# Performance work log

Hardware: AMD Instinct MI355X
Metric: run time of the kernel (lower is better)

Reference implementation:

```python
import jax, jax.numpy as jnp
import numpy as np
import math

H = 8
D_MODEL = 512
D_K = D_MODEL // H
NEG = -1.0e9


def setup_inputs() -> dict:
    key = jax.random.key(0)
    ks = jax.random.split(key, 10)
    B, S, D = 8, 1024, D_MODEL
    s = 1.0 / math.sqrt(D)
    return {
        "query": jax.random.normal(ks[0], (B, S, D), jnp.float32),
        "key": jax.random.normal(ks[1], (B, S, D), jnp.float32),
        "value": jax.random.normal(ks[2], (B, S, D), jnp.float32),
        "group_prob": jax.random.uniform(ks[3], (B, S, S), jnp.float32),
        "Wq": jax.random.normal(ks[4], (D, D), jnp.float32) * s,
        "Wk": jax.random.normal(ks[5], (D, D), jnp.float32) * s,
        "Wv": jax.random.normal(ks[6], (D, D), jnp.float32) * s,
        "Wh": jax.random.normal(ks[7], (D, D), jnp.float32) * s,
        "bh": jax.random.normal(ks[8], (D,), jnp.float32) * s,
        "mask": jax.random.randint(ks[9], (B, S, S), 0, 2, jnp.int32),
    }


def reference(query, key, value, group_prob, Wq, Wk, Wv, Wh, bh, mask):
    B, S, D = query.shape
    # project and split heads: [B, H, S, d_k]
    def split(x, W):
        return (x @ W.T).reshape(B, S, H, D_K).transpose(0, 2, 1, 3)
    q, k, v = split(query, Wq), split(key, Wk), split(value, Wv)
    scores = jnp.einsum('bhqd,bhkd->bhqk', q, k) / jnp.sqrt(jnp.asarray(D_K, q.dtype))
    # masked_fill where (mask | eye) == 0, i.e. keep mask-allowed or diagonal positions
    eye = jnp.eye(S, dtype=jnp.int32)
    allowed = (mask[:, None, :, :] | eye[None, None, :, :]) != 0  # [B,1,S,S]
    scores = jnp.where(allowed, scores, jnp.asarray(NEG, scores.dtype))
    p_attn = jax.nn.softmax(scores, axis=-1)
    p_attn = p_attn * group_prob[:, None, :, :]  # post-softmax group scaling
    x = jnp.einsum('bhqk,bhkd->bhqd', p_attn, v)
    x = x.transpose(0, 2, 1, 3).reshape(B, S, D)
    return x @ Wh.T + bh
```

## Files before the change

### kernel.cpp

```cpp
#include <hip/hip_runtime.h>
#include <hip/hip_bf16.h>
#include <cstdint>


typedef __attribute__((ext_vector_type(8))) short short8;
typedef __attribute__((ext_vector_type(4))) float f32x4;

__device__ __forceinline__ ushort f2bf(float x) {
    union { __hip_bfloat16 h; ushort u; } v;
    v.h = __float2bfloat16(x);
    return v.u;
}
__device__ __forceinline__ float bf2f(ushort u) {
    union { uint u; float f; } v; v.u = ((uint)u) << 16; return v.f;
}
__device__ __forceinline__ uint cvtpk(float lo, float hi) {
    uint r;
    asm("v_cvt_pk_bf16_f32 %0, %1, %2" : "=v"(r) : "v"(lo), "v"(hi));
    return r;
}
__device__ __forceinline__ f32x4 mfma16(short8 a, short8 b, f32x4 c) {
    return __builtin_amdgcn_mfma_f32_16x16x32_bf16(a, b, c, 0, 0, 0);
}
__device__ __forceinline__ void gl16(const void* g, const void* l) {
    __builtin_amdgcn_global_load_lds(
        (const __attribute__((address_space(1))) uint32_t*)(uintptr_t)g,
        (__attribute__((address_space(3))) uint32_t*)(uint32_t)(uintptr_t)l,
        16, 0, 0);
}

__global__ __launch_bounds__(256)
void prep(const float* __restrict__ q, const float* __restrict__ k,
          const float* __restrict__ v,
          const float* __restrict__ wq, const float* __restrict__ wk,
          const float* __restrict__ wv, const float* __restrict__ wh,
          const int* __restrict__ mask, const float* __restrict__ gp,
          ushort* __restrict__ qb, ushort* __restrict__ kb,
          ushort* __restrict__ vb,
          ushort* __restrict__ wqb, ushort* __restrict__ wkb,
          ushort* __restrict__ wvb, ushort* __restrict__ whb,
          ushort* __restrict__ gmb)
{
    const int bid = blockIdx.x, tid = threadIdx.x;
    if (bid < 8192) {
        size_t i = ((size_t)bid * 256 + tid) * 4;
        int4 m = *(const int4*)(mask + i);
        float4 gg = *(const float4*)(gp + i);
        int kk = (int)(i & 1023), qq = (int)((i >> 10) & 1023);
        uint u01 = cvtpk(gg.x, gg.y), u23 = cvtpk(gg.z, gg.w);
        ushort4 o;
        o.x = (m.x != 0 || qq == kk + 0) ? (ushort)(u01 & 0xffff) : (ushort)0xBF80;
        o.y = (m.y != 0 || qq == kk + 1) ? (ushort)(u01 >> 16)    : (ushort)0xBF80;
        o.z = (m.z != 0 || qq == kk + 2) ? (ushort)(u23 & 0xffff) : (ushort)0xBF80;
        o.w = (m.w != 0 || qq == kk + 3) ? (ushort)(u23 >> 16)    : (ushort)0xBF80;
        *(ushort4*)(gmb + i) = o;
    } else if (bid < 20480) {
        size_t id = ((size_t)(bid - 8192) * 256 + tid) * 4;
        int t = (int)(id >> 22);
        size_t off = id & 4194303;
        const float* s = (t == 0) ? q : (t == 1) ? k : v;
        ushort* d = (t == 0) ? qb : (t == 1) ? kb : vb;
        float4 x = *(const float4*)(s + off);
        uint2 o; o.x = cvtpk(x.x, x.y); o.y = cvtpk(x.z, x.w);
        *(uint2*)(d + off) = o;
    } else {
        size_t id = ((size_t)(bid - 20480) * 256 + tid) * 4;
        int t = (int)(id >> 18);
        size_t off = id & 262143;
        const float* s = (t == 0) ? wq : (t == 1) ? wk : (t == 2) ? wv : wh;
        ushort* d = (t == 0) ? wqb : (t == 1) ? wkb : (t == 2) ? wvb : whb;
        float4 x = *(const float4*)(s + off);
        uint2 o; o.x = cvtpk(x.x, x.y); o.y = cvtpk(x.z, x.w);
        *(uint2*)(d + off) = o;
    }
}

__global__ __launch_bounds__(256, 2)
void gemm3(const ushort* __restrict__ qb, const ushort* __restrict__ kb,
           const ushort* __restrict__ vb,
           const ushort* __restrict__ Wqb, const ushort* __restrict__ Wkb,
           const ushort* __restrict__ Wvb,
           ushort* __restrict__ q_ws, ushort* __restrict__ k_ws,
           ushort* __restrict__ vT)
{
    __shared__ __attribute__((aligned(16))) ushort As[8192];
    __shared__ __attribute__((aligned(16))) ushort Bs[8192];

    const int z = blockIdx.z;
    const ushort* A = (z == 0) ? qb : (z == 1) ? kb : Wvb;
    const ushort* B = (z == 0) ? Wqb : (z == 1) ? Wkb : vb;
    const int mt = (z == 2) ? blockIdx.y : blockIdx.x;
    const int nt = (z == 2) ? blockIdx.x : blockIdx.y;
    const int m0 = mt * 128, n0 = nt * 128;
    const int tid = threadIdx.x, lane = tid & 63, wave = tid >> 6;
    const int l15 = lane & 15, g = lane >> 4;
    const int wm = wave >> 1, wn = wave & 1;

    const int cb = (lane & 7) << 4;
    int soff[4];
    #pragma unroll
    for (int it = 0; it < 4; ++it) {
        int r = (it * 4 + wave) * 8 + (lane >> 3);
        soff[it] = r * 1024 + (cb ^ ((r & 7) << 4));
    }
    const char* Ab = (const char*)A + (size_t)m0 * 1024;
    const char* Bb = (const char*)B + (size_t)n0 * 1024;

    const int sw = (l15 & 7) << 4;
    const int c0 = (g * 16) ^ sw;
    const int c1 = (64 + g * 16) ^ sw;

    f32x4 acc[4][4];
    #pragma unroll
    for (int i = 0; i < 4; ++i)
        #pragma unroll
        for (int j = 0; j < 4; ++j) acc[i][j] = (f32x4){0.f, 0.f, 0.f, 0.f};

    for (int ks = 0; ks < 8; ++ks) {
        const int kof = ks * 128;
        #pragma unroll
        for (int it = 0; it < 4; ++it) {
            gl16(Ab + soff[it] + kof, (const char*)As + (it * 4 + wave) * 1024);
            gl16(Bb + soff[it] + kof, (const char*)Bs + (it * 4 + wave) * 1024);
        }
        __syncthreads();
        #pragma unroll
        for (int kk = 0; kk < 2; ++kk) {
            const int cc = kk ? c1 : c0;
            short8 af[4], bf[4];
            #pragma unroll
            for (int i = 0; i < 4; ++i)
                af[i] = *(const short8*)((const char*)As + (wm * 64 + i * 16 + l15) * 128 + cc);
            #pragma unroll
            for (int j = 0; j < 4; ++j)
                bf[j] = *(const short8*)((const char*)Bs + (wn * 64 + j * 16 + l15) * 128 + cc);
            #pragma unroll
            for (int i = 0; i < 4; ++i)
                #pragma unroll
                for (int j = 0; j < 4; ++j)
                    acc[i][j] = mfma16(af[i], bf[j], acc[i][j]);
        }
        __syncthreads();
    }

    #pragma unroll
    for (int i = 0; i < 4; ++i) {
        #pragma unroll
        for (int j = 0; j < 4; ++j) {
            #pragma unroll
            for (int r = 0; r < 4; ++r) {
                int mm = m0 + wm * 64 + i * 16 + g * 4 + r;
                int nn = n0 + wn * 64 + j * 16 + l15;
                float val = acc[i][j][r];
                if (z == 0) {
                    val *= 0.18033688f;
                    int b = mm >> 10, s = mm & 1023, h = nn >> 6, dk = nn & 63;
                    q_ws[((((size_t)(b * 8 + h)) << 10) + s) * 64 + dk] = f2bf(val);
                } else if (z == 1) {
                    int b = mm >> 10, s = mm & 1023, h = nn >> 6, dk = nn & 63;
                    k_ws[((((size_t)(b * 8 + h)) << 10) + s) * 64 + dk] = f2bf(val);
                } else {
                    int h = mm >> 6, d = mm & 63, b = nn >> 10, s = nn & 1023;
                    vT[(((size_t)(b * 8 + h) * 64 + d) << 10) + s] = f2bf(val);
                }
            }
        }
    }
}

__global__ __launch_bounds__(256, 2)
void gemm_o(const ushort* __restrict__ Xh, const ushort* __restrict__ Whb,
            const float* __restrict__ bias, float* __restrict__ out)
{
    __shared__ __attribute__((aligned(16))) ushort As[8192];
    __shared__ __attribute__((aligned(16))) ushort Bs[8192];

    const int m0 = blockIdx.x * 128, n0 = blockIdx.y * 128;
    const int tid = threadIdx.x, lane = tid & 63, wave = tid >> 6;
    const int l15 = lane & 15, g = lane >> 4;
    const int wm = wave >> 1, wn = wave & 1;
    const int bb = m0 >> 10, s0 = m0 & 1023;

    const int cb = (lane & 7) << 4;
    int aoff[4], boff[4];
    #pragma unroll
    for (int it = 0; it < 4; ++it) {
        int r = (it * 4 + wave) * 8 + (lane >> 3);
        int swz = cb ^ ((r & 7) << 4);
        aoff[it] = ((bb * 8) * 1024 + s0 + r) * 128 + swz;
        boff[it] = (n0 + r) * 1024 + swz;
    }
    const int sw = (l15 & 7) << 4;
    const int c0 = (g * 16) ^ sw;
    const int c1 = (64 + g * 16) ^ sw;

    f32x4 acc[4][4];
    #pragma unroll
    for (int i = 0; i < 4; ++i)
        #pragma unroll
        for (int j = 0; j < 4; ++j) acc[i][j] = (f32x4){0.f, 0.f, 0.f, 0.f};

    for (int ks = 0; ks < 8; ++ks) {
        #pragma unroll
        for (int it = 0; it < 4; ++it) {
            gl16((const char*)Xh + aoff[it] + ks * 131072,
                 (const char*)As + (it * 4 + wave) * 1024);
            gl16((const char*)Whb + boff[it] + ks * 128,
                 (const char*)Bs + (it * 4 + wave) * 1024);
        }
        __syncthreads();
        #pragma unroll
        for (int kk = 0; kk < 2; ++kk) {
            const int cc = kk ? c1 : c0;
            short8 af[4], bf[4];
            #pragma unroll
            for (int i = 0; i < 4; ++i)
                af[i] = *(const short8*)((const char*)As + (wm * 64 + i * 16 + l15) * 128 + cc);
            #pragma unroll
            for (int j = 0; j < 4; ++j)
                bf[j] = *(const short8*)((const char*)Bs + (wn * 64 + j * 16 + l15) * 128 + cc);
            #pragma unroll
            for (int i = 0; i < 4; ++i)
                #pragma unroll
                for (int j = 0; j < 4; ++j)
                    acc[i][j] = mfma16(af[i], bf[j], acc[i][j]);
        }
        __syncthreads();
    }

    float bv[4];
    #pragma unroll
    for (int j = 0; j < 4; ++j) bv[j] = bias[n0 + wn * 64 + j * 16 + l15];

    #pragma unroll
    for (int i = 0; i < 4; ++i)
        #pragma unroll
        for (int j = 0; j < 4; ++j)
            #pragma unroll
            for (int r = 0; r < 4; ++r) {
                int mm = m0 + wm * 64 + i * 16 + g * 4 + r;
                int nn = n0 + wn * 64 + j * 16 + l15;
                out[(size_t)mm * 512 + nn] = acc[i][j][r] + bv[j];
            }
}

__device__ __forceinline__ void softmax16(const short8 gc0, const short8 gc1,
                                          const f32x4 (&s4)[4], float& lsum,
                                          uint4& u0, uint4& u1)
{
    float p[16], gv[16];
    #pragma unroll
    for (int c = 0; c < 2; ++c) {
        const short8 gc = c ? gc1 : gc0;
        #pragma unroll
        for (int j = 0; j < 8; ++j) {
            const int jj = c * 8 + j;
            const int t4 = 2 * c + (j >> 2), r = j & 3;
            float gvv = bf2f((ushort)gc[j]);
            gv[jj] = gvv;
            p[jj] = exp2f((gvv >= 0.f) ? s4[t4][r] : -1.0e9f);
        }
    }
    lsum += (((p[0] + p[1]) + (p[2] + p[3])) + ((p[4] + p[5]) + (p[6] + p[7])))
          + (((p[8] + p[9]) + (p[10] + p[11])) + ((p[12] + p[13]) + (p[14] + p[15])));
    u0.x = cvtpk(p[0] * gv[0],  p[1] * gv[1]);
    u0.y = cvtpk(p[2] * gv[2],  p[3] * gv[3]);
    u0.z = cvtpk(p[4] * gv[4],  p[5] * gv[5]);
    u0.w = cvtpk(p[6] * gv[6],  p[7] * gv[7]);
    u1.x = cvtpk(p[8] * gv[8],  p[9] * gv[9]);
    u1.y = cvtpk(p[10] * gv[10], p[11] * gv[11]);
    u1.z = cvtpk(p[12] * gv[12], p[13] * gv[13]);
    u1.w = cvtpk(p[14] * gv[14], p[15] * gv[15]);
}

#define TILE_BODY(T, CUR, GCA0, GCA1, GCB0, GCB1, GNA0, GNA1, GNB0, GNB1)      \
  do {                                                                         \
    if ((T) < 15) {                                                            \
        GNA0 = *(const short8*)(gmpA + ((T) + 1) * 64 + g * 8);                \
        GNA1 = *(const short8*)(gmpA + ((T) + 1) * 64 + 32 + g * 8);           \
        GNB0 = *(const short8*)(gmpB + ((T) + 1) * 64 + g * 8);                \
        GNB1 = *(const short8*)(gmpB + ((T) + 1) * 64 + 32 + g * 8);           \
        const char* kp_ = Kpb + (size_t)((T) + 1) * 8192;                      \
        const char* vp_ = Vpb + (size_t)((T) + 1) * 128;                       \
        char* kd_ = (char*)&kv[(CUR) ^ 1][0][0] + wave * 4096;                 \
        char* vd_ = (char*)&kv[(CUR) ^ 1][1][0] + wave * 4096;                 \
        _Pragma("unroll")                                                      \
        for (int i_ = 0; i_ < 4; ++i_) {                                       \
            gl16(kp_ + koff[i_], kd_ + i_ * 1024);                             \
            gl16(vp_ + voff[i_], vd_ + i_ * 1024);                             \
        }                                                                      \
        asm volatile("s_waitcnt vmcnt(12)" ::: "memory");                      \
    } else {                                                                   \
        asm volatile("s_waitcnt vmcnt(0)" ::: "memory");                       \
    }                                                                          \
    __builtin_amdgcn_s_barrier();                                              \
    __builtin_amdgcn_sched_barrier(0);                                         \
    {                                                                          \
        const char* kbuf_ = (const char*)&kv[CUR][0][0];                       \
        const char* vbuf_ = (const char*)&kv[CUR][1][0];                       \
        f32x4 sA_[4], sB_[4];                                                  \
        __builtin_amdgcn_s_setprio(1);                                         \
        _Pragma("unroll")                                                      \
        for (int t4_ = 0; t4_ < 4; ++t4_) {                                    \
            const char* ka_ = kbuf_ + (t4_ * 16 + l15) * 128;                  \
            short8 k0_ = *(const short8*)(ka_ + c0);                           \
            short8 k1_ = *(const short8*)(ka_ + c1);                           \
            f32x4 za_ = (f32x4){0.f, 0.f, 0.f, 0.f};                           \
            za_ = mfma16(k0_, qa0, za_);                                       \
            za_ = mfma16(k1_, qa1, za_);                                       \
            sA_[t4_] = za_;                                                    \
            f32x4 zb_ = (f32x4){0.f, 0.f, 0.f, 0.f};                           \
            zb_ = mfma16(k0_, qb0, zb_);                                       \
            zb_ = mfma16(k1_, qb1, zb_);                                       \
            sB_[t4_] = zb_;                                                    \
        }                                                                      \
        __builtin_amdgcn_s_setprio(0);                                         \
        union { uint4 u; short8 s; } paA0_, paA1_, paB0_, paB1_;               \
        softmax16(GCA0, GCA1, sA_, lsA, paA0_.u, paA1_.u);                     \
        softmax16(GCB0, GCB1, sB_, lsB, paB0_.u, paB1_.u);                     \
        __builtin_amdgcn_s_setprio(1);                                         \
        _Pragma("unroll")                                                      \
        for (int td_ = 0; td_ < 4; ++td_) {                                    \
            const char* va_ = vbuf_ + (td_ * 16 + l15) * 128;                  \
            short8 v0_ = *(const short8*)(va_ + c0);                           \
            short8 v1_ = *(const short8*)(va_ + c1);                           \
            otA[td_] = mfma16(v0_, paA0_.s, otA[td_]);                         \
            otA[td_] = mfma16(v1_, paA1_.s, otA[td_]);                         \
            otB[td_] = mfma16(v0_, paB0_.s, otB[td_]);                         \
            otB[td_] = mfma16(v1_, paB1_.s, otB[td_]);                         \
        }                                                                      \
        __builtin_amdgcn_s_setprio(0);                                         \
    }                                                                          \
    __builtin_amdgcn_s_barrier();                                              \
  } while (0)

__global__ __launch_bounds__(128, 2)
void attn(const ushort* __restrict__ Qh, const ushort* __restrict__ Kh,
          const ushort* __restrict__ Vt, const ushort* __restrict__ gm,
          ushort* __restrict__ xo)
{
    __shared__ __attribute__((aligned(16))) ushort kv[2][2][4096];

    const int w = blockIdx.x;
    const int bh = w & 63, qt = w >> 6;
    const int tid = threadIdx.x, wave = tid >> 6, lane = tid & 63;
    const int l15 = lane & 15, g = lane >> 4;
    const int q0 = qt * 64 + wave * 32;
    const int b = bh >> 3;

    const char* Kpb = (const char*)(Kh + (size_t)bh * 65536);
    const char* Vpb = (const char*)(Vt + (size_t)bh * 65536);
    const ushort* QpA = Qh + ((size_t)bh * 1024 + q0 + l15) * 64;
    const ushort* QpB = QpA + 1024;
    const ushort* gmpA = gm + ((size_t)b * 1024 + q0 + l15) * 1024;
    const ushort* gmpB = gmpA + 16384;

    const short8 qa0 = *(const short8*)(QpA + g * 8);
    const short8 qa1 = *(const short8*)(QpA + 32 + g * 8);
    const short8 qb0 = *(const short8*)(QpB + g * 8);
    const short8 qb1 = *(const short8*)(QpB + 32 + g * 8);

    const int cbk = ((lane & 7) << 4) ^ ((lane >> 3) << 4);
    int koff[4], voff[4];
    #pragma unroll
    for (int i = 0; i < 4; ++i) {
        int p = (wave * 4 + i) * 8 + (lane >> 3);
        int gk = (p & 3) + 4 * ((p >> 4) & 1) + 8 * ((p >> 2) & 3) + 32 * (p >> 5);
        koff[i] = gk * 128 + cbk;
        voff[i] = p * 2048 + cbk;
    }

    const int sw = (l15 & 7) << 4;
    const int c0 = (g * 16) ^ sw;
    const int c1 = (64 + g * 16) ^ sw;

    f32x4 otA[4], otB[4];
    #pragma unroll
    for (int t = 0; t < 4; ++t) {
        otA[t] = (f32x4){0.f, 0.f, 0.f, 0.f};
        otB[t] = (f32x4){0.f, 0.f, 0.f, 0.f};
    }
    float lsA = 0.f, lsB = 0.f;

    short8 gEA0 = *(const short8*)(gmpA + g * 8);
    short8 gEA1 = *(const short8*)(gmpA + 32 + g * 8);
    short8 gEB0 = *(const short8*)(gmpB + g * 8);
    short8 gEB1 = *(const short8*)(gmpB + 32 + g * 8);
    short8 gOA0, gOA1, gOB0, gOB1;
    {
        char* kd = (char*)&kv[0][0][0] + wave * 4096;
        char* vd = (char*)&kv[0][1][0] + wave * 4096;
        #pragma unroll
        for (int i = 0; i < 4; ++i) {
            gl16(Kpb + koff[i], kd + i * 1024);
            gl16(Vpb + voff[i], vd + i * 1024);
        }
    }

    for (int tt = 0; tt < 16; tt += 2) {
        TILE_BODY(tt,     0, gEA0, gEA1, gEB0, gEB1, gOA0, gOA1, gOB0, gOB1);
        TILE_BODY(tt + 1, 1, gOA0, gOA1, gOB0, gOB1, gEA0, gEA1, gEB0, gEB1);
    }

    lsA += __shfl_xor(lsA, 16, 64);
    lsA += __shfl_xor(lsA, 32, 64);
    lsB += __shfl_xor(lsB, 16, 64);
    lsB += __shfl_xor(lsB, 32, 64);
    const float invA = 1.0f / lsA;
    const float invB = 1.0f / lsB;

    ushort* xpA = xo + ((size_t)bh * 1024 + q0 + l15) * 64;
    ushort* xpB = xpA + 1024;
    #pragma unroll
    for (int td = 0; td < 4; ++td) {
        uint2 oa, ob;
        oa.x = cvtpk(otA[td][0] * invA, otA[td][1] * invA);
        oa.y = cvtpk(otA[td][2] * invA, otA[td][3] * invA);
        ob.x = cvtpk(otB[td][0] * invB, otB[td][1] * invB);
        ob.y = cvtpk(otB[td][2] * invB, otB[td][3] * invB);
        *(uint2*)(xpA + td * 16 + g * 4) = oa;
        *(uint2*)(xpB + td * 16 + g * 4) = ob;
    }
}

extern "C" void kernel_launch(void* const* d_in, const int* in_sizes, int n_in,
                              void* d_out, int out_size, void* d_ws, size_t ws_size,
                              hipStream_t stream)
{
    const float* query = (const float*)d_in[0];
    const float* key   = (const float*)d_in[1];
    const float* value = (const float*)d_in[2];
    const float* gprob = (const float*)d_in[3];
    const float* Wq    = (const float*)d_in[4];
    const float* Wk    = (const float*)d_in[5];
    const float* Wv    = (const float*)d_in[6];
    const float* Wh    = (const float*)d_in[7];
    const float* bh    = (const float*)d_in[8];
    const int*   mask  = (const int*)d_in[9];
    float* out = (float*)d_out;

    ushort* ws = (ushort*)d_ws;
    const size_t HS = (size_t)64 * 65536;
    ushort* q_ws = ws;
    ushort* k_ws = ws + HS;
    ushort* vT   = ws + 2 * HS;
    ushort* gmb  = ws + 3 * HS;
    ushort* qb   = ws + 5 * HS;
    ushort* kb   = ws + 6 * HS;
    ushort* vb   = ws + 7 * HS;
    ushort* wqb  = ws + 8 * HS;
    ushort* wkb  = wqb + 262144;
    ushort* wvb  = wkb + 262144;
    ushort* whb  = wvb + 262144;
    ushort* x_ws = qb;

    prep<<<21504, 256, 0, stream>>>(query, key, value, Wq, Wk, Wv, Wh,
                                    mask, gprob, qb, kb, vb,
                                    wqb, wkb, wvb, whb, gmb);
    gemm3<<<dim3(64, 4, 3), 256, 0, stream>>>(qb, kb, vb, wqb, wkb, wvb,
                                              q_ws, k_ws, vT);
    attn<<<1024, 128, 0, stream>>>(q_ws, k_ws, vT, gmb, x_ws);
    gemm_o<<<dim3(64, 4), 256, 0, stream>>>(x_ws, whb, bh, out);
}
```

Baseline: 104.8 us.

## Drop LDS staging in attention; load K/V tiles directly into registers

The attention kernel no longer stages K and V tiles through double-buffered shared memory with async global-to-LDS copies and barriers. Each wave now loads its K fragments (register double-buffered one tile ahead) and V fragments straight from global memory into registers. Blocks grow to four waves covering 128 queries, with half as many blocks. This removes LDS traffic and block-wide barriers, at the cost of each wave fetching K/V independently through L1/L2, less coalesced loads, and higher register pressure.

```diff
diff --git a/kernel.cpp b/kernel.cpp
--- a/kernel.cpp
+++ b/kernel.cpp
@@ -273,106 +273,84 @@
     u1.w = cvtpk(p[14] * gv[14], p[15] * gv[15]);
 }
 
-#define TILE_BODY(T, CUR, GCA0, GCA1, GCB0, GCB1, GNA0, GNA1, GNB0, GNB1)      \
+#define LOADK(T, KD)                                                           \
+    _Pragma("unroll")                                                          \
+    for (int t4_ = 0; t4_ < 4; ++t4_) {                                        \
+        const ushort* kp_ = kbase + (size_t)(T) * 4096                         \
+                            + (t4_ & 1) * 256 + (t4_ >> 1) * 2048;             \
+        KD[2 * t4_]     = *(const short8*)kp_;                                 \
+        KD[2 * t4_ + 1] = *(const short8*)(kp_ + 32);                          \
+    }
+
+#define LOADG(T, GD)                                                           \
+    do {                                                                       \
+        GD[0] = *(const short8*)(gma + (T) * 64);                              \
+        GD[1] = *(const short8*)(gma + (T) * 64 + 32);                         \
+        GD[2] = *(const short8*)(gmb2 + (T) * 64);                             \
+        GD[3] = *(const short8*)(gmb2 + (T) * 64 + 32);                        \
+    } while (0)
+
+#define TILEB(T, KC, GC, KN, GN)                                               \
   do {                                                                         \
-    if ((T) < 15) {                                                            \
-        GNA0 = *(const short8*)(gmpA + ((T) + 1) * 64 + g * 8);                \
-        GNA1 = *(const short8*)(gmpA + ((T) + 1) * 64 + 32 + g * 8);           \
-        GNB0 = *(const short8*)(gmpB + ((T) + 1) * 64 + g * 8);                \
-        GNB1 = *(const short8*)(gmpB + ((T) + 1) * 64 + 32 + g * 8);           \
-        const char* kp_ = Kpb + (size_t)((T) + 1) * 8192;                      \
-        const char* vp_ = Vpb + (size_t)((T) + 1) * 128;                       \
-        char* kd_ = (char*)&kv[(CUR) ^ 1][0][0] + wave * 4096;                 \
-        char* vd_ = (char*)&kv[(CUR) ^ 1][1][0] + wave * 4096;                 \
-        _Pragma("unroll")                                                      \
-        for (int i_ = 0; i_ < 4; ++i_) {                                       \
-            gl16(kp_ + koff[i_], kd_ + i_ * 1024);                             \
-            gl16(vp_ + voff[i_], vd_ + i_ * 1024);                             \
-        }                                                                      \
-        asm volatile("s_waitcnt vmcnt(12)" ::: "memory");                      \
-    } else {                                                                   \
-        asm volatile("s_waitcnt vmcnt(0)" ::: "memory");                       \
+    f32x4 sA_[4], sB_[4];                                                      \
+    _Pragma("unroll")                                                          \
+    for (int t4_ = 0; t4_ < 4; ++t4_) {                                        \
+        f32x4 za_ = (f32x4){0.f, 0.f, 0.f, 0.f};                               \
+        za_ = mfma16(KC[2 * t4_], qa0, za_);                                   \
+        za_ = mfma16(KC[2 * t4_ + 1], qa1, za_);                               \
+        sA_[t4_] = za_;                                                        \
+        f32x4 zb_ = (f32x4){0.f, 0.f, 0.f, 0.f};                               \
+        zb_ = mfma16(KC[2 * t4_], qb0, zb_);                                   \
+        zb_ = mfma16(KC[2 * t4_ + 1], qb1, zb_);                               \
+        sB_[t4_] = zb_;                                                        \
     }                                                                          \
-    __builtin_amdgcn_s_barrier();                                              \
-    __builtin_amdgcn_sched_barrier(0);                                         \
-    {                                                                          \
-        const char* kbuf_ = (const char*)&kv[CUR][0][0];                       \
-        const char* vbuf_ = (const char*)&kv[CUR][1][0];                       \
-        f32x4 sA_[4], sB_[4];                                                  \
-        __builtin_amdgcn_s_setprio(1);                                         \
-        _Pragma("unroll")                                                      \
-        for (int t4_ = 0; t4_ < 4; ++t4_) {                                    \
-            const char* ka_ = kbuf_ + (t4_ * 16 + l15) * 128;                  \
-            short8 k0_ = *(const short8*)(ka_ + c0);                           \
-            short8 k1_ = *(const short8*)(ka_ + c1);                           \
-            f32x4 za_ = (f32x4){0.f, 0.f, 0.f, 0.f};                           \
-            za_ = mfma16(k0_, qa0, za_);                                       \
-            za_ = mfma16(k1_, qa1, za_);                                       \
-            sA_[t4_] = za_;                                                    \
-            f32x4 zb_ = (f32x4){0.f, 0.f, 0.f, 0.f};                           \
-            zb_ = mfma16(k0_, qb0, zb_);                                       \
-            zb_ = mfma16(k1_, qb1, zb_);                                       \
-            sB_[t4_] = zb_;                                                    \
-        }                                                                      \
-        __builtin_amdgcn_s_setprio(0);                                         \
-        union { uint4 u; short8 s; } paA0_, paA1_, paB0_, paB1_;               \
-        softmax16(GCA0, GCA1, sA_, lsA, paA0_.u, paA1_.u);                     \
-        softmax16(GCB0, GCB1, sB_, lsB, paB0_.u, paB1_.u);                     \
-        __builtin_amdgcn_s_setprio(1);                                         \
-        _Pragma("unroll")                                                      \
-        for (int td_ = 0; td_ < 4; ++td_) {                                    \
-            const char* va_ = vbuf_ + (td_ * 16 + l15) * 128;                  \
-            short8 v0_ = *(const short8*)(va_ + c0);                           \
-            short8 v1_ = *(const short8*)(va_ + c1);                           \
-            otA[td_] = mfma16(v0_, paA0_.s, otA[td_]);                         \
-            otA[td_] = mfma16(v1_, paA1_.s, otA[td_]);                         \
-            otB[td_] = mfma16(v0_, paB0_.s, otB[td_]);                         \
-            otB[td_] = mfma16(v1_, paB1_.s, otB[td_]);                         \
-        }                                                                      \
-        __builtin_amdgcn_s_setprio(0);                                         \
+    short8 vv_[8];                                                             \
+    _Pragma("unroll")                                                          \
+    for (int td_ = 0; td_ < 4; ++td_) {                                        \
+        const ushort* vp_ = vbase + td_ * 16384 + (T) * 64;                    \
+        vv_[2 * td_]     = *(const short8*)vp_;                                \
+        vv_[2 * td_ + 1] = *(const short8*)(vp_ + 32);                         \
     }                                                                          \
-    __builtin_amdgcn_s_barrier();                                              \
+    if ((T) < 15) { LOADK((T) + 1, KN); LOADG((T) + 1, GN); }                  \
+    union { uint4 u; short8 s; } paA0_, paA1_, paB0_, paB1_;                   \
+    softmax16(GC[0], GC[1], sA_, lsA, paA0_.u, paA1_.u);                       \
+    softmax16(GC[2], GC[3], sB_, lsB, paB0_.u, paB1_.u);                       \
+    _Pragma("unroll")                                                          \
+    for (int td_ = 0; td_ < 4; ++td_) {                                        \
+        otA[td_] = mfma16(vv_[2 * td_], paA0_.s, otA[td_]);                    \
+        otA[td_] = mfma16(vv_[2 * td_ + 1], paA1_.s, otA[td_]);                \
+        otB[td_] = mfma16(vv_[2 * td_], paB0_.s, otB[td_]);                    \
+        otB[td_] = mfma16(vv_[2 * td_ + 1], paB1_.s, otB[td_]);                \
+    }                                                                          \
   } while (0)
 
-__global__ __launch_bounds__(128, 2)
+__global__ __launch_bounds__(256, 2)
 void attn(const ushort* __restrict__ Qh, const ushort* __restrict__ Kh,
           const ushort* __restrict__ Vt, const ushort* __restrict__ gm,
           ushort* __restrict__ xo)
 {
-    __shared__ __attribute__((aligned(16))) ushort kv[2][2][4096];
-
     const int w = blockIdx.x;
     const int bh = w & 63, qt = w >> 6;
     const int tid = threadIdx.x, wave = tid >> 6, lane = tid & 63;
     const int l15 = lane & 15, g = lane >> 4;
-    const int q0 = qt * 64 + wave * 32;
+    const int q0 = qt * 128 + wave * 32;
     const int b = bh >> 3;
 
-    const char* Kpb = (const char*)(Kh + (size_t)bh * 65536);
-    const char* Vpb = (const char*)(Vt + (size_t)bh * 65536);
+    const ushort* Kp = Kh + (size_t)bh * 65536;
+    const ushort* Vp = Vt + (size_t)bh * 65536;
     const ushort* QpA = Qh + ((size_t)bh * 1024 + q0 + l15) * 64;
     const ushort* QpB = QpA + 1024;
-    const ushort* gmpA = gm + ((size_t)b * 1024 + q0 + l15) * 1024;
-    const ushort* gmpB = gmpA + 16384;
+    const ushort* gma  = gm + ((size_t)b * 1024 + q0 + l15) * 1024 + g * 8;
+    const ushort* gmb2 = gma + 16384;
 
     const short8 qa0 = *(const short8*)(QpA + g * 8);
     const short8 qa1 = *(const short8*)(QpA + 32 + g * 8);
     const short8 qb0 = *(const short8*)(QpB + g * 8);
     const short8 qb1 = *(const short8*)(QpB + 32 + g * 8);
 
-    const int cbk = ((lane & 7) << 4) ^ ((lane >> 3) << 4);
-    int koff[4], voff[4];
-    #pragma unroll
-    for (int i = 0; i < 4; ++i) {
-        int p = (wave * 4 + i) * 8 + (lane >> 3);
-        int gk = (p & 3) + 4 * ((p >> 4) & 1) + 8 * ((p >> 2) & 3) + 32 * (p >> 5);
-        koff[i] = gk * 128 + cbk;
-        voff[i] = p * 2048 + cbk;
-    }
-
-    const int sw = (l15 & 7) << 4;
-    const int c0 = (g * 16) ^ sw;
-    const int c1 = (64 + g * 16) ^ sw;
+    const int krb = 8 * (l15 >> 2) + (l15 & 3);
+    const ushort* kbase = Kp + (size_t)krb * 64 + g * 8;
+    const ushort* vbase = Vp + ((size_t)l15 << 10) + g * 8;
 
     f32x4 otA[4], otB[4];
     #pragma unroll
@@ -382,24 +360,13 @@
     }
     float lsA = 0.f, lsB = 0.f;
 
-    short8 gEA0 = *(const short8*)(gmpA + g * 8);
-    short8 gEA1 = *(const short8*)(gmpA + 32 + g * 8);
-    short8 gEB0 = *(const short8*)(gmpB + g * 8);
-    short8 gEB1 = *(const short8*)(gmpB + 32 + g * 8);
-    short8 gOA0, gOA1, gOB0, gOB1;
-    {
-        char* kd = (char*)&kv[0][0][0] + wave * 4096;
-        char* vd = (char*)&kv[0][1][0] + wave * 4096;
-        #pragma unroll
-        for (int i = 0; i < 4; ++i) {
-            gl16(Kpb + koff[i], kd + i * 1024);
-            gl16(Vpb + voff[i], vd + i * 1024);
-        }
-    }
+    short8 kE[8], kO[8], gE[4], gO[4];
+    LOADK(0, kE);
+    LOADG(0, gE);
 
     for (int tt = 0; tt < 16; tt += 2) {
-        TILE_BODY(tt,     0, gEA0, gEA1, gEB0, gEB1, gOA0, gOA1, gOB0, gOB1);
-        TILE_BODY(tt + 1, 1, gOA0, gOA1, gOB0, gOB1, gEA0, gEA1, gEB0, gEB1);
+        TILEB(tt,     kE, gE, kO, gO);
+        TILEB(tt + 1, kO, gO, kE, gE);
     }
 
     lsA += __shfl_xor(lsA, 16, 64);
@@ -459,6 +426,6 @@
                                     wqb, wkb, wvb, whb, gmb);
     gemm3<<<dim3(64, 4, 3), 256, 0, stream>>>(qb, kb, vb, wqb, wkb, wvb,
                                               q_ws, k_ws, vT);
-    attn<<<1024, 128, 0, stream>>>(q_ws, k_ws, vT, gmb, x_ws);
+    attn<<<512, 256, 0, stream>>>(q_ws, k_ws, vT, gmb, x_ws);
     gemm_o<<<dim3(64, 4), 256, 0, stream>>>(x_ws, whb, bh, out);
 }
```

Measured after the change: 134.5 us. 1.28x slower.
